# Optimization experiments

Hardware: AMD Instinct MI355X
Metric: run time of the kernel (lower is better)

Reference implementation:

```python
import jax, jax.numpy as jnp
import numpy as np

NUM_NODES = 100000
EMB_DIM = 256
HID_DIM = 256
NUM_REL = 500
NUM_EDGES = 250000


def setup_inputs() -> dict:
    key = jax.random.key(0)
    ks = jax.random.split(key, 6)
    x = jax.random.normal(ks[0], (NUM_NODES, EMB_DIM), dtype=jnp.float32)
    edge_index = jax.random.randint(ks[1], (2, NUM_EDGES), 0, NUM_NODES, dtype=jnp.int64)
    edge_type = jax.random.randint(ks[2], (NUM_EDGES,), 0, NUM_REL, dtype=jnp.int64)
    # nn.Linear weights: shape [out, in]; _init_weights -> normal(0,1), bias zero
    W_head = jax.random.normal(ks[3], (HID_DIM, EMB_DIM), dtype=jnp.float32)
    b_head = jnp.zeros((HID_DIM,), dtype=jnp.float32)
    W_tail = jax.random.normal(ks[4], (HID_DIM, EMB_DIM), dtype=jnp.float32)
    b_tail = jnp.zeros((HID_DIM,), dtype=jnp.float32)
    rel_emb = jax.random.normal(ks[5], (NUM_REL, HID_DIM), dtype=jnp.float32)
    return {"x": x, "edge_index": edge_index, "edge_type": edge_type,
            "W_head": W_head, "b_head": b_head,
            "W_tail": W_tail, "b_tail": b_tail, "rel_emb": rel_emb}


def reference(x, edge_index, edge_type, W_head, b_head, W_tail, b_tail, rel_emb):
    # gcn == 'no' branch of DistMultNet.forward
    h_head = x[edge_index[0]] @ W_head.T + b_head          # [E, H]
    h_tail = x[edge_index[1]] @ W_tail.T + b_tail          # [E, H]
    h_rel = rel_emb[edge_type]                             # [E, H]
    scores = jnp.sum(h_head * h_rel * h_tail, axis=1)      # [E]
    return jax.nn.sigmoid(scores)
```

## Files before the change

kernel.cpp:

```cpp
#include <hip/hip_runtime.h>
#include <math.h>

#define EMB 256

typedef _Float16 half8 __attribute__((ext_vector_type(8)));
typedef float f32x4 __attribute__((ext_vector_type(4)));

__device__ __forceinline__ void gload_lds16(const void* gsrc, void* lds) {
    __builtin_amdgcn_global_load_lds(
        (const __attribute__((address_space(1))) void*)gsrc,
        (__attribute__((address_space(3))) void*)lds,
        16, 0, 0);
}

__device__ __forceinline__ void split8(const f32x4 a, const f32x4 b,
                                       half8& hi, half8& lo) {
#pragma unroll
    for (int i = 0; i < 4; ++i) {
        hi[i]     = (_Float16)a[i];
        lo[i]     = (_Float16)(a[i] - (float)hi[i]);
        hi[4 + i] = (_Float16)b[i];
        lo[4 + i] = (_Float16)(b[i] - (float)hi[4 + i]);
    }
}

__global__ void presplit_w(const float* __restrict__ Wh, const float* __restrict__ Wt,
                           _Float16* __restrict__ Whs, _Float16* __restrict__ Wts)
{
    const int g = blockIdx.x * 256 + threadIdx.x;
    const int m = g >> 5;
    const int cs = g & 31;
    const int c = cs >> 2, seg = cs & 3;
    const float* src = (m < 256) ? Wh : Wt;
    _Float16* dst    = (m < 256) ? Whs : Wts;
    const int r = m & 255;

    const float* s = src + (size_t)r * EMB + c * 32 + seg * 8;
    const f32x4 v0 = *(const f32x4*)s;
    const f32x4 v1 = *(const f32x4*)(s + 4);
    half8 hi, lo;
    split8(v0, v1, hi, lo);
    _Float16* d = dst + (size_t)r * 512 + c * 64;
    const int sw = r & 7;
    *(half8*)(d + ((seg       ^ sw) << 3)) = hi;
    *(half8*)(d + (((4 + seg) ^ sw) << 3)) = lo;
}

__global__ __launch_bounds__(256, 2)
void gemm_dual(const float* __restrict__ X,
               const _Float16* __restrict__ Whs, const _Float16* __restrict__ Wts,
               const float* __restrict__ bh, const float* __restrict__ bt,
               float* __restrict__ Hout, float* __restrict__ Tout,
               int M, int nwg)
{
    __shared__ __align__(16) _Float16 Ax[128 * 64];
    __shared__ __align__(16) _Float16 Bh[128 * 64];
    __shared__ __align__(16) _Float16 Bt[128 * 64];

    const int fl = blockIdx.x;
    const int q = nwg >> 3, r = nwg & 7;
    const int xcd = fl & 7, ix = fl >> 3;
    const int wg = (xcd < r) ? xcd * (q + 1) + ix
                             : r * (q + 1) + (xcd - r) * q + ix;
    const int n0 = (wg & 1) << 7;
    const int m0 = (wg >> 1) << 7;

    const int tid = threadIdx.x;
    const int lane = tid & 63;
    const int wv = tid >> 6;
    const int wm = (wv >> 1) << 6;
    const int wn = (wv & 1) << 6;
    const int l15 = lane & 15, l4 = lane >> 4;

    const int ar = tid >> 1;
    const int ahalf = tid & 1;
    const int gmA = m0 + ar;
    const float* aSrc = X + (size_t)(gmA < M ? gmA : M - 1) * EMB + ahalf * 16;
    char* aDst = (char*)Ax + ar * 128;
    const int ar7 = ar & 7;
    const int s0 = ahalf * 2, s1 = s0 + 1;
    const int oh0 = ((s0       ^ ar7) << 4), ol0 = (((4 + s0) ^ ar7) << 4);
    const int oh1 = ((s1       ^ ar7) << 4), ol1 = (((4 + s1) ^ ar7) << 4);

    const int brow = tid >> 3, bg = tid & 7;
    const char* bhSrc = (const char*)Whs + (size_t)(n0 + brow) * 1024 + bg * 16;
    const char* btSrc = (const char*)Wts + (size_t)(n0 + brow) * 1024 + bg * 16;
    char* bhDst = (char*)Bh + brow * 128 + bg * 16;
    char* btDst = (char*)Bt + brow * 128 + bg * 16;

    f32x4 accH[4][4], accT[4][4];
#pragma unroll
    for (int i = 0; i < 4; ++i)
#pragma unroll
        for (int j = 0; j < 4; ++j) {
            accH[i][j] = (f32x4){0.f, 0.f, 0.f, 0.f};
            accT[i][j] = (f32x4){0.f, 0.f, 0.f, 0.f};
        }

    f32x4 xg[4];
#pragma unroll
    for (int p = 0; p < 4; ++p) xg[p] = *(const f32x4*)(aSrc + p * 4);

    for (int c = 0; c < 8; ++c) {
        if (c) __syncthreads();
        const int cb = c << 7;
#pragma unroll
        for (int i = 0; i < 4; ++i) {
            gload_lds16(bhSrc + (size_t)i * 32768 + cb, bhDst + i * 4096);
            gload_lds16(btSrc + (size_t)i * 32768 + cb, btDst + i * 4096);
        }
        {
            half8 hi0, lo0, hi1, lo1;
            split8(xg[0], xg[1], hi0, lo0);
            split8(xg[2], xg[3], hi1, lo1);
            *(half8*)(aDst + oh0) = hi0;
            *(half8*)(aDst + ol0) = lo0;
            *(half8*)(aDst + oh1) = hi1;
            *(half8*)(aDst + ol1) = lo1;
        }
        __syncthreads();

        if (c < 7) {
            const float* an = aSrc + (c + 1) * 32;
#pragma unroll
            for (int p = 0; p < 4; ++p) xg[p] = *(const f32x4*)(an + p * 4);
        }

        half8 ahh[4], ahl[4];
#pragma unroll
        for (int fi = 0; fi < 4; ++fi) {
            const int row = wm + fi * 16 + l15;
            const char* rb = (const char*)Ax + row * 128;
            ahh[fi] = *(const half8*)(rb + (((l4    ) ^ (row & 7)) << 4));
            ahl[fi] = *(const half8*)(rb + (((l4 + 4) ^ (row & 7)) << 4));
        }
#pragma unroll
        for (int j = 0; j < 4; ++j) {
            const int n = wn + j * 16 + l15;
            const int n7 = n & 7;
            const char* hr = (const char*)Bh + n * 128;
            const char* tr = (const char*)Bt + n * 128;
            const half8 bhh = *(const half8*)(hr + (((l4    ) ^ n7) << 4));
            const half8 bhl = *(const half8*)(hr + (((l4 + 4) ^ n7) << 4));
            const half8 bth = *(const half8*)(tr + (((l4    ) ^ n7) << 4));
            const half8 btl = *(const half8*)(tr + (((l4 + 4) ^ n7) << 4));
#pragma unroll
            for (int i = 0; i < 4; ++i) {
                accH[i][j] = __builtin_amdgcn_mfma_f32_16x16x32_f16(ahh[i], bhh, accH[i][j], 0, 0, 0);
                accH[i][j] = __builtin_amdgcn_mfma_f32_16x16x32_f16(ahh[i], bhl, accH[i][j], 0, 0, 0);
                accH[i][j] = __builtin_amdgcn_mfma_f32_16x16x32_f16(ahl[i], bhh, accH[i][j], 0, 0, 0);
                accT[i][j] = __builtin_amdgcn_mfma_f32_16x16x32_f16(ahh[i], bth, accT[i][j], 0, 0, 0);
                accT[i][j] = __builtin_amdgcn_mfma_f32_16x16x32_f16(ahh[i], btl, accT[i][j], 0, 0, 0);
                accT[i][j] = __builtin_amdgcn_mfma_f32_16x16x32_f16(ahl[i], bth, accT[i][j], 0, 0, 0);
            }
        }
    }

    float bhv[4], btv[4];
#pragma unroll
    for (int j = 0; j < 4; ++j) {
        bhv[j] = bh[n0 + wn + j * 16 + l15];
        btv[j] = bt[n0 + wn + j * 16 + l15];
    }
#pragma unroll
    for (int i = 0; i < 4; ++i) {
        const int rbase = m0 + wm + i * 16 + l4 * 4;
#pragma unroll
        for (int rg = 0; rg < 4; ++rg) {
            const int gr = rbase + rg;
            if (gr < M) {
                float* dh = &Hout[(size_t)gr * EMB + n0 + wn];
                float* dt = &Tout[(size_t)gr * EMB + n0 + wn];
#pragma unroll
                for (int j = 0; j < 4; ++j) {
                    const int col = j * 16 + l15;
                    dh[col] = accH[i][j][rg] + bhv[j];
                    dt[col] = accT[i][j][rg] + btv[j];
                }
            }
        }
    }
}

__global__ __launch_bounds__(256)
void edge_score2(const float* __restrict__ H, const float* __restrict__ T,
                 const float* __restrict__ rel, const int* __restrict__ ei,
                 const int* __restrict__ et, float* __restrict__ out, int E)
{
    const int lane = threadIdx.x & 63;
    const int wid = threadIdx.x >> 6;
    const int e0 = (blockIdx.x * 4 + wid) * 2;
    if (e0 >= E) return;
    const bool two = (e0 + 1) < E;
    const int e1 = two ? e0 + 1 : e0;

    const int s0 = ei[e0], s1 = ei[e1];
    const int d0 = ei[E + e0], d1 = ei[E + e1];
    const int r0 = et[e0], r1 = et[e1];

    const int lo = lane * 4;
    const float4 h0 = *(const float4*)&H[(size_t)s0 * EMB + lo];
    const float4 h1 = *(const float4*)&H[(size_t)s1 * EMB + lo];
    const float4 t0 = *(const float4*)&T[(size_t)d0 * EMB + lo];
    const float4 t1 = *(const float4*)&T[(size_t)d1 * EMB + lo];
    const float4 g0 = *(const float4*)&rel[(size_t)r0 * EMB + lo];
    const float4 g1 = *(const float4*)&rel[(size_t)r1 * EMB + lo];

    float p0 = h0.x * g0.x * t0.x + h0.y * g0.y * t0.y
             + h0.z * g0.z * t0.z + h0.w * g0.w * t0.w;
    float p1 = h1.x * g1.x * t1.x + h1.y * g1.y * t1.y
             + h1.z * g1.z * t1.z + h1.w * g1.w * t1.w;
#pragma unroll
    for (int off = 32; off > 0; off >>= 1) {
        p0 += __shfl_xor(p0, off, 64);
        p1 += __shfl_xor(p1, off, 64);
    }
    if (lane == 0) {
        out[e0] = 1.0f / (1.0f + expf(-p0));
        if (two) out[e1] = 1.0f / (1.0f + expf(-p1));
    }
}

__global__ __launch_bounds__(256)
void edge_direct(const float* __restrict__ X, const int* __restrict__ ei,
                 const int* __restrict__ et,
                 const float* __restrict__ Wh, const float* __restrict__ bh,
                 const float* __restrict__ Wt, const float* __restrict__ bt,
                 const float* __restrict__ rel, float* __restrict__ out, int E)
{
    __shared__ float xsrc[EMB], xdst[EMB];
    __shared__ float red[256];
    const int e = blockIdx.x;
    const int tid = threadIdx.x;
    const int src = ei[e], dst = ei[E + e], r = et[e];

    xsrc[tid] = X[(size_t)src * EMB + tid];
    xdst[tid] = X[(size_t)dst * EMB + tid];
    __syncthreads();

    float ah = 0.f, at = 0.f;
    const float* wh = Wh + (size_t)tid * EMB;
    const float* wt = Wt + (size_t)tid * EMB;
#pragma unroll 8
    for (int k = 0; k < EMB; k += 4) {
        float4 w4 = *(const float4*)&wh[k];
        ah += w4.x * xsrc[k] + w4.y * xsrc[k + 1] + w4.z * xsrc[k + 2] + w4.w * xsrc[k + 3];
        float4 v4 = *(const float4*)&wt[k];
        at += v4.x * xdst[k] + v4.y * xdst[k + 1] + v4.z * xdst[k + 2] + v4.w * xdst[k + 3];
    }
    red[tid] = (ah + bh[tid]) * rel[(size_t)r * EMB + tid] * (at + bt[tid]);
    __syncthreads();
    for (int s2 = 128; s2 > 0; s2 >>= 1) {
        if (tid < s2) red[tid] += red[tid + s2];
        __syncthreads();
    }
    if (tid == 0) out[e] = 1.0f / (1.0f + expf(-red[0]));
}

extern "C" void kernel_launch(void* const* d_in, const int* in_sizes, int n_in,
                              void* d_out, int out_size, void* d_ws, size_t ws_size,
                              hipStream_t stream) {
    const float* x   = (const float*)d_in[0];
    const int*   ei  = (const int*)d_in[1];
    const int*   et  = (const int*)d_in[2];
    const float* Wh  = (const float*)d_in[3];
    const float* bh  = (const float*)d_in[4];
    const float* Wt  = (const float*)d_in[5];
    const float* bt  = (const float*)d_in[6];
    const float* rel = (const float*)d_in[7];
    float* out = (float*)d_out;

    const int M = in_sizes[0] / EMB;
    const int E = in_sizes[2];

    const size_t szHT = (size_t)2 * M * EMB * sizeof(float);
    const size_t szWs = (size_t)2 * 256 * 512 * sizeof(_Float16);

    if (ws_size >= szHT + szWs) {
        float* H = (float*)d_ws;
        float* T = H + (size_t)M * EMB;
        _Float16* Whs = (_Float16*)((char*)d_ws + szHT);
        _Float16* Wts = Whs + (size_t)256 * 512;

        presplit_w<<<64, 256, 0, stream>>>(Wh, Wt, Whs, Wts);
        const int mtiles = (M + 127) / 128;
        const int nwg = 2 * mtiles;
        gemm_dual<<<nwg, 256, 0, stream>>>(x, Whs, Wts, bh, bt, H, T, M, nwg);
        edge_score2<<<(E + 7) / 8, 256, 0, stream>>>(H, T, rel, ei, et, out, E);
    } else {
        edge_direct<<<E, 256, 0, stream>>>(x, ei, et, Wh, bh, Wt, bt, rel, out, E);
    }
}
```

Baseline: 179.4 us.

## Split dual GEMM into per-weight workgroups with double-buffered async LDS staging

Each workgroup now computes either the head or the tail projection instead of both, so the grid doubles and per-thread accumulator registers halve. X tiles are loaded as fp32 straight into LDS with async global-to-LDS loads, double-buffered so the next K-chunk loads while the current one runs MFMAs. The fp16 hi/lo split of X moves to the point where LDS fragments are read. In exchange, X is read from global memory twice (once per weight) and the split arithmetic is repeated per fragment read.

```diff
diff --git a/kernel.cpp b/kernel.cpp
--- a/kernel.cpp
+++ b/kernel.cpp
@@ -47,23 +47,27 @@
 }
 
 __global__ __launch_bounds__(256, 2)
-void gemm_dual(const float* __restrict__ X,
-               const _Float16* __restrict__ Whs, const _Float16* __restrict__ Wts,
-               const float* __restrict__ bh, const float* __restrict__ bt,
-               float* __restrict__ Hout, float* __restrict__ Tout,
-               int M, int nwg)
-{
-    __shared__ __align__(16) _Float16 Ax[128 * 64];
-    __shared__ __align__(16) _Float16 Bh[128 * 64];
-    __shared__ __align__(16) _Float16 Bt[128 * 64];
+void gemm_single(const float* __restrict__ X,
+                 const _Float16* __restrict__ Whs, const _Float16* __restrict__ Wts,
+                 const float* __restrict__ bh, const float* __restrict__ bt,
+                 float* __restrict__ Hout, float* __restrict__ Tout,
+                 int M, int nwg)
+{
+    __shared__ __align__(16) float    Af[2][128 * 32];
+    __shared__ __align__(16) _Float16 Bf[2][128 * 64];
 
     const int fl = blockIdx.x;
     const int q = nwg >> 3, r = nwg & 7;
     const int xcd = fl & 7, ix = fl >> 3;
     const int wg = (xcd < r) ? xcd * (q + 1) + ix
                              : r * (q + 1) + (xcd - r) * q + ix;
-    const int n0 = (wg & 1) << 7;
-    const int m0 = (wg >> 1) << 7;
+    const int variant = wg & 3;
+    const int m0 = (wg >> 2) << 7;
+    const int n0 = (variant & 1) << 7;
+    const int sel = variant >> 1;
+    const _Float16* __restrict__ Ws = sel ? Wts : Whs;
+    const float* __restrict__ bias  = sel ? bt : bh;
+    float* __restrict__ OUT         = sel ? Tout : Hout;
 
     const int tid = threadIdx.x;
     const int lane = tid & 63;
@@ -72,96 +76,77 @@
     const int wn = (wv & 1) << 6;
     const int l15 = lane & 15, l4 = lane >> 4;
 
-    const int ar = tid >> 1;
-    const int ahalf = tid & 1;
-    const int gmA = m0 + ar;
-    const float* aSrc = X + (size_t)(gmA < M ? gmA : M - 1) * EMB + ahalf * 16;
-    char* aDst = (char*)Ax + ar * 128;
-    const int ar7 = ar & 7;
-    const int s0 = ahalf * 2, s1 = s0 + 1;
-    const int oh0 = ((s0       ^ ar7) << 4), ol0 = (((4 + s0) ^ ar7) << 4);
-    const int oh1 = ((s1       ^ ar7) << 4), ol1 = (((4 + s1) ^ ar7) << 4);
-
-    const int brow = tid >> 3, bg = tid & 7;
-    const char* bhSrc = (const char*)Whs + (size_t)(n0 + brow) * 1024 + bg * 16;
-    const char* btSrc = (const char*)Wts + (size_t)(n0 + brow) * 1024 + bg * 16;
-    char* bhDst = (char*)Bh + brow * 128 + bg * 16;
-    char* btDst = (char*)Bt + brow * 128 + bg * 16;
-
-    f32x4 accH[4][4], accT[4][4];
+    const int srow = tid >> 3;
+    const int sg = tid & 7;
+    int aSrcOff[4];
+    const char* bSrc0 = (const char*)Ws + (size_t)(n0 + srow) * 1024 + sg * 16;
+#pragma unroll
+    for (int i = 0; i < 4; ++i) {
+        const int row = srow + (i << 5);
+        aSrcOff[i] = (sg ^ (row & 7)) << 4;
+    }
+    const int ldOff = srow * 128 + sg * 16;
+
+    f32x4 acc[4][4];
 #pragma unroll
     for (int i = 0; i < 4; ++i)
 #pragma unroll
-        for (int j = 0; j < 4; ++j) {
-            accH[i][j] = (f32x4){0.f, 0.f, 0.f, 0.f};
-            accT[i][j] = (f32x4){0.f, 0.f, 0.f, 0.f};
-        }
-
-    f32x4 xg[4];
-#pragma unroll
-    for (int p = 0; p < 4; ++p) xg[p] = *(const f32x4*)(aSrc + p * 4);
+        for (int j = 0; j < 4; ++j) acc[i][j] = (f32x4){0.f, 0.f, 0.f, 0.f};
+
+    auto STAGE = [&](int b, int c) {
+        const int cb = c << 7;
+#pragma unroll
+        for (int i = 0; i < 4; ++i) {
+            const int row = srow + (i << 5);
+            const int gm = m0 + row;
+            const int gmc = gm < M ? gm : M - 1;
+            gload_lds16((const char*)X + (size_t)gmc * 1024 + cb + aSrcOff[i],
+                        (char*)&Af[b][0] + ldOff + (i << 12));
+            gload_lds16(bSrc0 + (size_t)i * 32768 + cb,
+                        (char*)&Bf[b][0] + ldOff + (i << 12));
+        }
+    };
+
+    STAGE(0, 0);
+    __syncthreads();
 
     for (int c = 0; c < 8; ++c) {
-        if (c) __syncthreads();
-        const int cb = c << 7;
-#pragma unroll
-        for (int i = 0; i < 4; ++i) {
-            gload_lds16(bhSrc + (size_t)i * 32768 + cb, bhDst + i * 4096);
-            gload_lds16(btSrc + (size_t)i * 32768 + cb, btDst + i * 4096);
-        }
-        {
-            half8 hi0, lo0, hi1, lo1;
-            split8(xg[0], xg[1], hi0, lo0);
-            split8(xg[2], xg[3], hi1, lo1);
-            *(half8*)(aDst + oh0) = hi0;
-            *(half8*)(aDst + ol0) = lo0;
-            *(half8*)(aDst + oh1) = hi1;
-            *(half8*)(aDst + ol1) = lo1;
-        }
-        __syncthreads();
-
-        if (c < 7) {
-            const float* an = aSrc + (c + 1) * 32;
-#pragma unroll
-            for (int p = 0; p < 4; ++p) xg[p] = *(const f32x4*)(an + p * 4);
-        }
+        const int buf = c & 1;
+        if (c < 7) STAGE(buf ^ 1, c + 1);
+
+        const char* Ab = (const char*)&Af[buf][0];
+        const char* Bb = (const char*)&Bf[buf][0];
 
         half8 ahh[4], ahl[4];
 #pragma unroll
         for (int fi = 0; fi < 4; ++fi) {
             const int row = wm + fi * 16 + l15;
-            const char* rb = (const char*)Ax + row * 128;
-            ahh[fi] = *(const half8*)(rb + (((l4    ) ^ (row & 7)) << 4));
-            ahl[fi] = *(const half8*)(rb + (((l4 + 4) ^ (row & 7)) << 4));
+            const char* rb = Ab + row * 128;
+            const f32x4 a0 = *(const f32x4*)(rb + (((l4 << 1)      ^ (row & 7)) << 4));
+            const f32x4 a1 = *(const f32x4*)(rb + ((((l4 << 1) | 1) ^ (row & 7)) << 4));
+            split8(a0, a1, ahh[fi], ahl[fi]);
         }
 #pragma unroll
         for (int j = 0; j < 4; ++j) {
             const int n = wn + j * 16 + l15;
             const int n7 = n & 7;
-            const char* hr = (const char*)Bh + n * 128;
-            const char* tr = (const char*)Bt + n * 128;
-            const half8 bhh = *(const half8*)(hr + (((l4    ) ^ n7) << 4));
-            const half8 bhl = *(const half8*)(hr + (((l4 + 4) ^ n7) << 4));
-            const half8 bth = *(const half8*)(tr + (((l4    ) ^ n7) << 4));
-            const half8 btl = *(const half8*)(tr + (((l4 + 4) ^ n7) << 4));
+            const char* nb = Bb + n * 128;
+            const half8 bhh = *(const half8*)(nb + (((l4    ) ^ n7) << 4));
+            const half8 bhl = *(const half8*)(nb + (((l4 + 4) ^ n7) << 4));
 #pragma unroll
             for (int i = 0; i < 4; ++i) {
-                accH[i][j] = __builtin_amdgcn_mfma_f32_16x16x32_f16(ahh[i], bhh, accH[i][j], 0, 0, 0);
-                accH[i][j] = __builtin_amdgcn_mfma_f32_16x16x32_f16(ahh[i], bhl, accH[i][j], 0, 0, 0);
-                accH[i][j] = __builtin_amdgcn_mfma_f32_16x16x32_f16(ahl[i], bhh, accH[i][j], 0, 0, 0);
-                accT[i][j] = __builtin_amdgcn_mfma_f32_16x16x32_f16(ahh[i], bth, accT[i][j], 0, 0, 0);
-                accT[i][j] = __builtin_amdgcn_mfma_f32_16x16x32_f16(ahh[i], btl, accT[i][j], 0, 0, 0);
-                accT[i][j] = __builtin_amdgcn_mfma_f32_16x16x32_f16(ahl[i], bth, accT[i][j], 0, 0, 0);
+                acc[i][j] = __builtin_amdgcn_mfma_f32_16x16x32_f16(ahh[i], bhh, acc[i][j], 0, 0, 0);
+                acc[i][j] = __builtin_amdgcn_mfma_f32_16x16x32_f16(ahh[i], bhl, acc[i][j], 0, 0, 0);
+                acc[i][j] = __builtin_amdgcn_mfma_f32_16x16x32_f16(ahl[i], bhh, acc[i][j], 0, 0, 0);
             }
         }
-    }
-
-    float bhv[4], btv[4];
-#pragma unroll
-    for (int j = 0; j < 4; ++j) {
-        bhv[j] = bh[n0 + wn + j * 16 + l15];
-        btv[j] = bt[n0 + wn + j * 16 + l15];
-    }
+        __syncthreads();
+    }
+
+    float bv[4];
+#pragma unroll
+    for (int j = 0; j < 4; ++j) bv[j] = bias[n0 + wn + j * 16 + l15];
+
 #pragma unroll
     for (int i = 0; i < 4; ++i) {
         const int rbase = m0 + wm + i * 16 + l4 * 4;
@@ -169,14 +154,10 @@
         for (int rg = 0; rg < 4; ++rg) {
             const int gr = rbase + rg;
             if (gr < M) {
-                float* dh = &Hout[(size_t)gr * EMB + n0 + wn];
-                float* dt = &Tout[(size_t)gr * EMB + n0 + wn];
-#pragma unroll
-                for (int j = 0; j < 4; ++j) {
-                    const int col = j * 16 + l15;
-                    dh[col] = accH[i][j][rg] + bhv[j];
-                    dt[col] = accT[i][j][rg] + btv[j];
-                }
+                float* dst = &OUT[(size_t)gr * EMB + n0 + wn];
+#pragma unroll
+                for (int j = 0; j < 4; ++j)
+                    dst[j * 16 + l15] = acc[i][j][rg] + bv[j];
             }
         }
     }
@@ -284,8 +265,8 @@
 
         presplit_w<<<64, 256, 0, stream>>>(Wh, Wt, Whs, Wts);
         const int mtiles = (M + 127) / 128;
-        const int nwg = 2 * mtiles;
-        gemm_dual<<<nwg, 256, 0, stream>>>(x, Whs, Wts, bh, bt, H, T, M, nwg);
+        const int nwg = 4 * mtiles;
+        gemm_single<<<nwg, 256, 0, stream>>>(x, Whs, Wts, bh, bt, H, T, M, nwg);
         edge_score2<<<(E + 7) / 8, 256, 0, stream>>>(H, T, rel, ei, et, out, E);
     } else {
         edge_direct<<<E, 256, 0, stream>>>(x, ei, et, Wh, bh, Wt, bt, rel, out, E);
```

Result: slower. 217.5 us (+21.2%).
